# Kernel optimization log

Hardware: AMD Instinct MI355X
Metric: run time of the kernel (lower is better)

Reference implementation:

```python
import jax, jax.numpy as jnp
import numpy as np

N = 100000
E = 1600000
D = 128      # input feature dim
H = 128      # hidden_channels
O = 2        # out_channels
NEG_SLOPE = 0.2
EPS = 1e-16  # PyG softmax denominator epsilon


def gat_conv(x, src, dst, W_src, W_dst, att_src, att_dst, bias):
    """PyG GATConv, heads=1, add_self_loops=False, concat=True."""
    xs = x @ W_src                      # [N, C]
    xd = x @ W_dst                      # [N, C]
    a_s = xs @ att_src                  # [N]
    a_d = xd @ att_dst                  # [N]
    e = jax.nn.leaky_relu(a_s[src] + a_d[dst], NEG_SLOPE)   # [E]
    # segment softmax over edges grouped by destination node
    m = jax.ops.segment_max(e, dst, num_segments=N)          # [N]
    m = jnp.where(jnp.isfinite(m), m, 0.0)
    ex = jnp.exp(e - m[dst])                                  # [E]
    denom = jax.ops.segment_sum(ex, dst, num_segments=N)      # [N]
    alpha = ex / (denom[dst] + EPS)                            # [E]
    msg = alpha[:, None] * xs[src]                             # [E, C]
    out = jax.ops.segment_sum(msg, dst, num_segments=N)       # [N, C]
    return out + bias


def setup_inputs() -> dict:
    key = jax.random.key(0)
    ks = jax.random.split(key, 14)
    s = lambda k, shape, fan: jax.random.normal(k, shape, jnp.float32) * (1.0 / np.sqrt(fan))
    x = jax.random.normal(ks[0], (N, D), jnp.float32)
    edge_index = jax.random.randint(ks[1], (2, E), 0, N, dtype=jnp.int32)
    return {
        "x": x,
        "edge_index": edge_index,
        "W1s": s(ks[2], (D, H), D), "W1d": s(ks[3], (D, H), D),
        "a1s": s(ks[4], (H,), H),   "a1d": s(ks[5], (H,), H),
        "b1": jnp.zeros((H,), jnp.float32),
        "W2s": s(ks[6], (H, H), H), "W2d": s(ks[7], (H, H), H),
        "a2s": s(ks[8], (H,), H),   "a2d": s(ks[9], (H,), H),
        "b2": jnp.zeros((H,), jnp.float32),
        "Wl": s(ks[10], (H, O), H), "bl": jnp.zeros((O,), jnp.float32),
    }


def reference(x, edge_index, W1s, W1d, a1s, a1d, b1, W2s, W2d, a2s, a2d, b2, Wl, bl):
    src, dst = edge_index[0], edge_index[1]
    h = jax.nn.relu(gat_conv(x, src, dst, W1s, W1d, a1s, a1d, b1))
    # dropout p=0.3 is identity at inference
    h = jax.nn.relu(gat_conv(h, src, dst, W2s, W2d, a2s, a2d, b2))
    return h @ Wl + bl  # [N, O]
```

## Files before the change

kernel.cpp:

```cpp
#include <hip/hip_runtime.h>
#include <hip/hip_fp16.h>

#define NBSHIFT 8
#define BSZ     256
#define CAP     5120
#define EBLK    8192

typedef _Float16 f16x8 __attribute__((ext_vector_type(8)));
typedef float    f32x4 __attribute__((ext_vector_type(4)));


#define GEMM_LDS_BYTES (128 * 136 * 2 + 512)

template <bool XHALF>
__device__ __forceinline__ void gemm_body(
        const void* __restrict__ Xv, const float* __restrict__ Ws,
        const float* __restrict__ Wd, const float* __restrict__ attd,
        const float* __restrict__ att,
        __half* __restrict__ Y, float* __restrict__ a_s, float* __restrict__ a_d,
        int N, int blk, char* smem) {
    _Float16 (*sWh)[136] = (_Float16(*)[136])smem;
    float* svd = (float*)(smem + 128 * 136 * 2);
    int t = threadIdx.x;

    if (t < 128) {
        const float4* wr = (const float4*)&Wd[t * 128];
        const float4* ar = (const float4*)attd;
        float s = 0.f;
#pragma unroll 8
        for (int j = 0; j < 32; j++) {
            float4 w = wr[j], a = ar[j];
            s += w.x * a.x + w.y * a.y + w.z * a.z + w.w * a.w;
        }
        svd[t] = s;
    }
#pragma unroll
    for (int i = 0; i < 16; i++) {
        int gid = t + i * 256;
        int n = gid & 127, kq = gid >> 7;
        _Float16 p[4];
        p[0] = (_Float16)Ws[(kq * 4 + 0) * 128 + n];
        p[1] = (_Float16)Ws[(kq * 4 + 1) * 128 + n];
        p[2] = (_Float16)Ws[(kq * 4 + 2) * 128 + n];
        p[3] = (_Float16)Ws[(kq * 4 + 3) * 128 + n];
        *(uint2*)&sWh[n][kq * 4] = *(uint2*)p;
    }
    __syncthreads();

    int l = t & 63, wv = t >> 6;
    int quad = l >> 4, lm = l & 15;
    int rbase = blk * 64 + wv * 16;
    int arow = rbase + lm;
    bool rok = arow < N;

    f32x4 acc[8];
#pragma unroll
    for (int c = 0; c < 8; c++) acc[c] = (f32x4){0.f, 0.f, 0.f, 0.f};
    float adp = 0.f;

#pragma unroll
    for (int kc = 0; kc < 4; kc++) {
        int k0 = kc * 32 + quad * 8;
        float xf[8];
        f16x8 af;
        if constexpr (XHALF) {
            const __half* xrow = (const __half*)Xv + (size_t)arow * 128;
            if (rok) {
                af = *(const f16x8*)&xrow[k0];
            } else {
#pragma unroll
                for (int j = 0; j < 8; j++) af[j] = (_Float16)0.f;
            }
#pragma unroll
            for (int j = 0; j < 8; j++) xf[j] = (float)af[j];
        } else {
            const float* xrow = (const float*)Xv + (size_t)arow * 128;
            if (rok) {
                *(float4*)&xf[0] = *(const float4*)&xrow[k0];
                *(float4*)&xf[4] = *(const float4*)&xrow[k0 + 4];
            } else {
#pragma unroll
                for (int j = 0; j < 8; j++) xf[j] = 0.f;
            }
#pragma unroll
            for (int j = 0; j < 8; j++) af[j] = (_Float16)xf[j];
        }
        float4 v0 = *(const float4*)&svd[k0];
        float4 v1 = *(const float4*)&svd[k0 + 4];
        adp += xf[0] * v0.x + xf[1] * v0.y + xf[2] * v0.z + xf[3] * v0.w
             + xf[4] * v1.x + xf[5] * v1.y + xf[6] * v1.z + xf[7] * v1.w;
#pragma unroll
        for (int c = 0; c < 8; c++) {
            f16x8 bf = *(const f16x8*)&sWh[c * 16 + lm][k0];
            acc[c] = __builtin_amdgcn_mfma_f32_16x16x32_f16(af, bf, acc[c], 0, 0, 0);
        }
    }

    adp += __shfl_xor(adp, 16);
    adp += __shfl_xor(adp, 32);
    if (quad == 0 && rok) a_d[arow] = adp;

    float attc[8];
#pragma unroll
    for (int c = 0; c < 8; c++) attc[c] = att[c * 16 + lm];
#pragma unroll
    for (int r = 0; r < 4; r++) {
        int grow = rbase + quad * 4 + r;
        bool gok = grow < N;
        float p = 0.f;
#pragma unroll
        for (int c = 0; c < 8; c++) {
            if (gok) Y[(size_t)grow * 128 + c * 16 + lm] = __float2half(acc[c][r]);
            p += acc[c][r] * attc[c];
        }
        p += __shfl_xor(p, 1); p += __shfl_xor(p, 2); p += __shfl_xor(p, 4); p += __shfl_xor(p, 8);
        if (lm == 0 && gok) a_s[grow] = p;
    }
}

__global__ __launch_bounds__(256, 4) void k_fuse1(
        const float* __restrict__ X, const float* __restrict__ W1s,
        const float* __restrict__ W1d, const float* __restrict__ a1d,
        const float* __restrict__ a1s,
        __half* __restrict__ Y, float* __restrict__ a_s, float* __restrict__ a_d, int N, int gb,
        const int* __restrict__ src, const int* __restrict__ dst, int E,
        int* __restrict__ cursor, unsigned* __restrict__ pairs) {
    __shared__ __align__(16) char smem[GEMM_LDS_BYTES];
    int t = threadIdx.x;

    if ((int)blockIdx.x >= gb) {
        int* hist  = (int*)smem;
        int* start = hist + 512;
        hist[t] = 0; hist[t + 256] = 0;
        __syncthreads();
        int e00 = ((int)blockIdx.x - gb) * EBLK;

#pragma unroll
        for (int ch = 0; ch < EBLK / 1024; ch++) {
            int e = e00 + ch * 1024 + t * 4;
            if (e + 3 < E) {
                int4 dv = *(const int4*)&dst[e];
                atomicAdd(&hist[dv.x >> NBSHIFT], 1);
                atomicAdd(&hist[dv.y >> NBSHIFT], 1);
                atomicAdd(&hist[dv.z >> NBSHIFT], 1);
                atomicAdd(&hist[dv.w >> NBSHIFT], 1);
            } else {
                for (int i = 0; i < 4; i++)
                    if (e + i < E) atomicAdd(&hist[dst[e + i] >> NBSHIFT], 1);
            }
        }
        __syncthreads();
        if (hist[t] > 0)       start[t]       = atomicAdd(&cursor[t],       hist[t]);
        if (hist[t + 256] > 0) start[t + 256] = atomicAdd(&cursor[t + 256], hist[t + 256]);
        __syncthreads();
        hist[t] = 0; hist[t + 256] = 0;
        __syncthreads();
#pragma unroll
        for (int ch = 0; ch < EBLK / 1024; ch++) {
            int e = e00 + ch * 1024 + t * 4;
            if (e + 3 < E) {
                int4 dv = *(const int4*)&dst[e];
                int4 sv = *(const int4*)&src[e];
                int b0 = dv.x >> NBSHIFT; int r0 = atomicAdd(&hist[b0], 1);
                pairs[b0 * CAP + start[b0] + r0] = ((unsigned)(dv.x & (BSZ - 1)) << 17) | (unsigned)sv.x;
                int b1 = dv.y >> NBSHIFT; int r1 = atomicAdd(&hist[b1], 1);
                pairs[b1 * CAP + start[b1] + r1] = ((unsigned)(dv.y & (BSZ - 1)) << 17) | (unsigned)sv.y;
                int b2 = dv.z >> NBSHIFT; int r2 = atomicAdd(&hist[b2], 1);
                pairs[b2 * CAP + start[b2] + r2] = ((unsigned)(dv.z & (BSZ - 1)) << 17) | (unsigned)sv.z;
                int b3 = dv.w >> NBSHIFT; int r3 = atomicAdd(&hist[b3], 1);
                pairs[b3 * CAP + start[b3] + r3] = ((unsigned)(dv.w & (BSZ - 1)) << 17) | (unsigned)sv.w;
            } else {
                for (int i = 0; i < 4; i++) {
                    if (e + i < E) {
                        int d = dst[e + i], s = src[e + i];
                        int b = d >> NBSHIFT;
                        int r = atomicAdd(&hist[b], 1);
                        pairs[b * CAP + start[b] + r] = ((unsigned)(d & (BSZ - 1)) << 17) | (unsigned)s;
                    }
                }
            }
        }
        return;
    }

    gemm_body<false>(X, W1s, W1d, a1d, a1s, Y, a_s, a_d, N, blockIdx.x, smem);
}

__global__ __launch_bounds__(256, 4) void k_gemm2(
        const __half* __restrict__ X, const float* __restrict__ W2s,
        const float* __restrict__ W2d, const float* __restrict__ a2d,
        const float* __restrict__ a2s,
        __half* __restrict__ Y, float* __restrict__ a_s, float* __restrict__ a_d, int N) {
    __shared__ __align__(16) char smem[GEMM_LDS_BYTES];
    gemm_body<true>(X, W2s, W2d, a2d, a2s, Y, a_s, a_d, N, blockIdx.x, smem);
}

__global__ __launch_bounds__(256) void kB_csr(const unsigned* __restrict__ pairs,
                                              const int* __restrict__ cursor,
                                              int* __restrict__ row_start, int* __restrict__ row_end,
                                              int* __restrict__ csr_src, int N) {
    __shared__ int cnt[BSZ];
    __shared__ int cur[BSZ];
    __shared__ int sS[256];
    int b = blockIdx.x, t = threadIdx.x;
    int base = b * CAP;
    int ecnt = cursor[b];
    int nodeBase = b << NBSHIFT;
    cnt[t] = 0;
    __syncthreads();
    for (int j = t; j < ecnt; j += 256)
        atomicAdd(&cnt[pairs[base + j] >> 17], 1);
    __syncthreads();
    int c0 = cnt[t];
    sS[t] = c0; __syncthreads();
    for (int off = 1; off < 256; off <<= 1) {
        int x = (t >= off) ? sS[t - off] : 0;
        __syncthreads();
        sS[t] += x;
        __syncthreads();
    }
    int excl = sS[t] - c0;
    cur[t] = excl;
    int g = nodeBase + t;
    if (g < N) { row_start[g] = base + excl; row_end[g] = base + excl + c0; }
    __syncthreads();
    for (int j = t; j < ecnt; j += 256) {
        unsigned p = pairs[base + j];
        int r = atomicAdd(&cur[p >> 17], 1);
        csr_src[base + r] = (int)(p & 0x1FFFFu);
    }
}


__device__ __forceinline__ void fma_mix2(float& a0, float& a1, unsigned h2, float w) {
    asm("v_fma_mix_f32 %0, %1, %2, %0 op_sel_hi:[1,0,0]" : "+v"(a0) : "v"(h2), "v"(w));
    asm("v_fma_mix_f32 %0, %1, %2, %0 op_sel:[1,0,0] op_sel_hi:[1,0,0]" : "+v"(a1) : "v"(h2), "v"(w));
}

#define ACC_MIX(u, wj)  do {                                    \
    const unsigned* _w32 = (const unsigned*)&(u);               \
    fma_mix2(acc[0], acc[1], _w32[0], (wj));                    \
    fma_mix2(acc[2], acc[3], _w32[1], (wj));                    \
    fma_mix2(acc[4], acc[5], _w32[2], (wj));                    \
    fma_mix2(acc[6], acc[7], _w32[3], (wj));                    \
} while (0)

template <bool HEAD>
__global__ __launch_bounds__(256, 6) void k_agg(const int* __restrict__ csr_src, const int* __restrict__ rs_,
                                                const int* __restrict__ re_,
                                                const float* __restrict__ a_s, const float* __restrict__ a_d,
                                                const __half* __restrict__ xs, const float* __restrict__ bias,
                                                const float* __restrict__ Wl, const float* __restrict__ bl,
                                                void* __restrict__ outv, int N) {
    __shared__ int2 sP[4][4][16];
    int t = threadIdx.x; int wv = t >> 6, l = t & 63;
    int q = l >> 4, es = l & 15;
    int n = blockIdx.x * 16 + wv * 4 + q;
    bool nok = n < N;
    int rs0 = 0, deg = 0;
    if (nok) { rs0 = rs_[n]; deg = re_[n] - rs0; }
    float adn = nok ? a_d[n] : 0.f;
    const int* cs = csr_src + rs0;
    int c = es * 8;

    int R = (deg + 15) >> 4;
    R = max(R, __shfl_xor(R, 16));
    R = max(R, __shfl_xor(R, 32));

    float acc[8];
#pragma unroll
    for (int k = 0; k < 8; k++) acc[k] = 0.f;
    float dnl = 0.f;
    int2 (*sq)[16] = sP[wv];

    for (int r = 0; r < R; ++r) {
        int i = r * 16 + es;
        int idx = 0; float w = 0.f;
        if (i < deg) {
            idx = cs[i];
            float tv = a_s[idx] + adn;
            tv = tv > 0.f ? tv : 0.2f * tv;
            w = __expf(tv);
        }
        dnl += w;
        sq[q][es] = make_int2(idx, __float_as_int(w));

        int rem = deg - r * 16;
        int mcq = rem >= 16 ? 16 : (rem > 0 ? ((rem + 3) & ~3) : 0);
        const int2* spq = sq[q];
        for (int e = 0; e < mcq; e += 4) {
            int4 pA = *(const int4*)&spq[e];
            int4 pB = *(const int4*)&spq[e + 2];
            uint4 u0 = *(const uint4*)&xs[(size_t)pA.x * 128 + c];
            uint4 u1 = *(const uint4*)&xs[(size_t)pA.z * 128 + c];
            uint4 u2 = *(const uint4*)&xs[(size_t)pB.x * 128 + c];
            uint4 u3 = *(const uint4*)&xs[(size_t)pB.z * 128 + c];
            ACC_MIX(u0, __int_as_float(pA.y));
            ACC_MIX(u1, __int_as_float(pA.w));
            ACC_MIX(u2, __int_as_float(pB.y));
            ACC_MIX(u3, __int_as_float(pB.w));
        }
    }

    dnl += __shfl_xor(dnl, 1);
    dnl += __shfl_xor(dnl, 2);
    dnl += __shfl_xor(dnl, 4);
    dnl += __shfl_xor(dnl, 8);
    float inv = 1.f / (dnl + 1e-16f);

    float hv[8];
    float4 b0 = *(const float4*)&bias[c];
    float4 b1 = *(const float4*)&bias[c + 4];
    float bb[8] = {b0.x, b0.y, b0.z, b0.w, b1.x, b1.y, b1.z, b1.w};
#pragma unroll
    for (int k = 0; k < 8; k++) {
        float v = acc[k] * inv + bb[k];
        hv[k] = v > 0.f ? v : 0.f;
    }

    if (HEAD) {
        float p0 = 0.f, p1 = 0.f;
#pragma unroll
        for (int k = 0; k < 8; k++) {
            p0 += hv[k] * Wl[2 * (c + k)];
            p1 += hv[k] * Wl[2 * (c + k) + 1];
        }
        p0 += __shfl_xor(p0, 1); p0 += __shfl_xor(p0, 2);
        p0 += __shfl_xor(p0, 4); p0 += __shfl_xor(p0, 8);
        p1 += __shfl_xor(p1, 1); p1 += __shfl_xor(p1, 2);
        p1 += __shfl_xor(p1, 4); p1 += __shfl_xor(p1, 8);
        if (es == 0 && nok) {
            float* out = (float*)outv;
            out[2 * n]     = p0 + bl[0];
            out[2 * n + 1] = p1 + bl[1];
        }
    } else {
        if (nok) {
            __half* hout = (__half*)outv;
            __half hb[8];
#pragma unroll
            for (int k = 0; k < 8; k++) hb[k] = __float2half(hv[k]);
            *(uint4*)&hout[(size_t)n * 128 + c] = *(uint4*)hb;
        }
    }
}


extern "C" void kernel_launch(void* const* d_in, const int* in_sizes, int n_in,
                              void* d_out, int out_size, void* d_ws, size_t ws_size,
                              hipStream_t stream) {
    const float* x   = (const float*)d_in[0];
    const int*   ei  = (const int*)d_in[1];
    const float* W1s = (const float*)d_in[2];
    const float* W1d = (const float*)d_in[3];
    const float* a1s = (const float*)d_in[4];
    const float* a1d = (const float*)d_in[5];
    const float* b1  = (const float*)d_in[6];
    const float* W2s = (const float*)d_in[7];
    const float* W2d = (const float*)d_in[8];
    const float* a2s = (const float*)d_in[9];
    const float* a2d = (const float*)d_in[10];
    const float* b2  = (const float*)d_in[11];
    const float* Wl  = (const float*)d_in[12];
    const float* bl  = (const float*)d_in[13];
    float* out = (float*)d_out;

    int N = in_sizes[0] / 128;
    int E = in_sizes[1] / 2;
    const int* srcA = ei;
    const int* dstA = ei + E;
    int NB = (N + BSZ - 1) >> NBSHIFT;

    __half* xs = (__half*)d_ws;
    __half* h  = xs + (size_t)N * 128;
    float* as_ = (float*)(h + (size_t)N * 128);
    float* ad_ = as_ + N;
    int* row_start = (int*)(ad_ + N);
    int* row_end   = row_start + N;
    int* csr_src   = row_end + N;
    int* cursor    = csr_src + (size_t)NB * CAP;
    unsigned* pairs = (unsigned*)h;

    int gb = (N + 63) / 64;
    int EB = (E + EBLK - 1) / EBLK;
    int ab = (N + 15) / 16;

    hipMemsetAsync(cursor, 0, (size_t)NB * 4, stream);

    k_fuse1<<<gb + EB, 256, 0, stream>>>(x, W1s, W1d, a1d, a1s, xs, as_, ad_, N, gb,
                                         srcA, dstA, E, cursor, pairs);

    kB_csr<<<NB, 256, 0, stream>>>(pairs, cursor, row_start, row_end, csr_src, N);

    k_agg<false><<<ab, 256, 0, stream>>>(csr_src, row_start, row_end, as_, ad_, xs, b1, nullptr, nullptr, h, N);

    k_gemm2<<<gb, 256, 0, stream>>>(h, W2s, W2d, a2d, a2s, xs, as_, ad_, N);

    k_agg<true><<<ab, 256, 0, stream>>>(csr_src, row_start, row_end, as_, ad_, xs, b2, Wl, bl, out, N);
}
```

Before: 313.5 us.

## Split binning from GEMM1, prefetch GEMM inputs, unroll aggregation gathers

```diff
diff --git a/kernel.cpp b/kernel.cpp
--- a/kernel.cpp
+++ b/kernel.cpp
@@ -9,8 +9,17 @@
 typedef _Float16 f16x8 __attribute__((ext_vector_type(8)));
 typedef float    f32x4 __attribute__((ext_vector_type(4)));
 
-
 #define GEMM_LDS_BYTES (128 * 136 * 2 + 512)
+
+__device__ __forceinline__ f16x8 cvt_dot8(float4 x0, float4 x1, const float* sv, float& adp) {
+    f16x8 a;
+    a[0] = (_Float16)x0.x; a[1] = (_Float16)x0.y; a[2] = (_Float16)x0.z; a[3] = (_Float16)x0.w;
+    a[4] = (_Float16)x1.x; a[5] = (_Float16)x1.y; a[6] = (_Float16)x1.z; a[7] = (_Float16)x1.w;
+    float4 v0 = *(const float4*)sv, v1 = *(const float4*)(sv + 4);
+    adp += x0.x * v0.x + x0.y * v0.y + x0.z * v0.z + x0.w * v0.w
+         + x1.x * v1.x + x1.y * v1.y + x1.z * v1.z + x1.w * v1.w;
+    return a;
+}
 
 template <bool XHALF>
 __device__ __forceinline__ void gemm_body(
@@ -22,6 +31,35 @@
     _Float16 (*sWh)[136] = (_Float16(*)[136])smem;
     float* svd = (float*)(smem + 128 * 136 * 2);
     int t = threadIdx.x;
+    int l = t & 63, wv = t >> 6;
+    int quad = l >> 4, lm = l & 15;
+    int rbase = blk * 64 + wv * 16;
+    int arow = rbase + lm;
+    bool rok = arow < N;
+
+    float4 xf[8];
+    f16x8  xh[4];
+    if constexpr (XHALF) {
+        const f16x8* xr = (const f16x8*)((const __half*)Xv + (size_t)arow * 128 + quad * 8);
+        if (rok) { xh[0] = xr[0]; xh[1] = xr[4]; xh[2] = xr[8]; xh[3] = xr[12]; }
+        else {
+#pragma unroll
+            for (int kc = 0; kc < 4; kc++)
+#pragma unroll
+                for (int j = 0; j < 8; j++) xh[kc][j] = (_Float16)0.f;
+        }
+    } else {
+        const float4* xr = (const float4*)((const float*)Xv + (size_t)arow * 128 + quad * 8);
+        if (rok) {
+            xf[0] = xr[0];  xf[1] = xr[1];
+            xf[2] = xr[8];  xf[3] = xr[9];
+            xf[4] = xr[16]; xf[5] = xr[17];
+            xf[6] = xr[24]; xf[7] = xr[25];
+        } else {
+#pragma unroll
+            for (int j = 0; j < 8; j++) xf[j] = make_float4(0.f, 0.f, 0.f, 0.f);
+        }
+    }
 
     if (t < 128) {
         const float4* wr = (const float4*)&Wd[t * 128];
@@ -47,52 +85,33 @@
     }
     __syncthreads();
 
-    int l = t & 63, wv = t >> 6;
-    int quad = l >> 4, lm = l & 15;
-    int rbase = blk * 64 + wv * 16;
-    int arow = rbase + lm;
-    bool rok = arow < N;
+    float adp = 0.f;
+    f16x8 af[4];
+    if constexpr (XHALF) {
+#pragma unroll
+        for (int kc = 0; kc < 4; kc++) {
+            af[kc] = xh[kc];
+            const float* sv = &svd[kc * 32 + quad * 8];
+#pragma unroll
+            for (int j = 0; j < 8; j++) adp += (float)xh[kc][j] * sv[j];
+        }
+    } else {
+        af[0] = cvt_dot8(xf[0], xf[1], &svd[0  + quad * 8], adp);
+        af[1] = cvt_dot8(xf[2], xf[3], &svd[32 + quad * 8], adp);
+        af[2] = cvt_dot8(xf[4], xf[5], &svd[64 + quad * 8], adp);
+        af[3] = cvt_dot8(xf[6], xf[7], &svd[96 + quad * 8], adp);
+    }
 
     f32x4 acc[8];
 #pragma unroll
     for (int c = 0; c < 8; c++) acc[c] = (f32x4){0.f, 0.f, 0.f, 0.f};
-    float adp = 0.f;
-
 #pragma unroll
     for (int kc = 0; kc < 4; kc++) {
         int k0 = kc * 32 + quad * 8;
-        float xf[8];
-        f16x8 af;
-        if constexpr (XHALF) {
-            const __half* xrow = (const __half*)Xv + (size_t)arow * 128;
-            if (rok) {
-                af = *(const f16x8*)&xrow[k0];
-            } else {
-#pragma unroll
-                for (int j = 0; j < 8; j++) af[j] = (_Float16)0.f;
-            }
-#pragma unroll
-            for (int j = 0; j < 8; j++) xf[j] = (float)af[j];
-        } else {
-            const float* xrow = (const float*)Xv + (size_t)arow * 128;
-            if (rok) {
-                *(float4*)&xf[0] = *(const float4*)&xrow[k0];
-                *(float4*)&xf[4] = *(const float4*)&xrow[k0 + 4];
-            } else {
-#pragma unroll
-                for (int j = 0; j < 8; j++) xf[j] = 0.f;
-            }
-#pragma unroll
-            for (int j = 0; j < 8; j++) af[j] = (_Float16)xf[j];
-        }
-        float4 v0 = *(const float4*)&svd[k0];
-        float4 v1 = *(const float4*)&svd[k0 + 4];
-        adp += xf[0] * v0.x + xf[1] * v0.y + xf[2] * v0.z + xf[3] * v0.w
-             + xf[4] * v1.x + xf[5] * v1.y + xf[6] * v1.z + xf[7] * v1.w;
 #pragma unroll
         for (int c = 0; c < 8; c++) {
             f16x8 bf = *(const f16x8*)&sWh[c * 16 + lm][k0];
-            acc[c] = __builtin_amdgcn_mfma_f32_16x16x32_f16(af, bf, acc[c], 0, 0, 0);
+            acc[c] = __builtin_amdgcn_mfma_f32_16x16x32_f16(af[kc], bf, acc[c], 0, 0, 0);
         }
     }
 
@@ -118,71 +137,69 @@
     }
 }
 
-__global__ __launch_bounds__(256, 4) void k_fuse1(
+__global__ __launch_bounds__(256) void k_bin(
+        const int* __restrict__ src, const int* __restrict__ dst, int E,
+        int* __restrict__ cursor, unsigned* __restrict__ pairs) {
+    __shared__ int hist[512];
+    __shared__ int start[512];
+    int t = threadIdx.x;
+    hist[t] = 0; hist[t + 256] = 0;
+    __syncthreads();
+    int e00 = (int)blockIdx.x * EBLK;
+
+#pragma unroll
+    for (int ch = 0; ch < EBLK / 1024; ch++) {
+        int e = e00 + ch * 1024 + t * 4;
+        if (e + 3 < E) {
+            int4 dv = *(const int4*)&dst[e];
+            atomicAdd(&hist[dv.x >> NBSHIFT], 1);
+            atomicAdd(&hist[dv.y >> NBSHIFT], 1);
+            atomicAdd(&hist[dv.z >> NBSHIFT], 1);
+            atomicAdd(&hist[dv.w >> NBSHIFT], 1);
+        } else {
+            for (int i = 0; i < 4; i++)
+                if (e + i < E) atomicAdd(&hist[dst[e + i] >> NBSHIFT], 1);
+        }
+    }
+    __syncthreads();
+    if (hist[t] > 0)       start[t]       = atomicAdd(&cursor[t],       hist[t]);
+    if (hist[t + 256] > 0) start[t + 256] = atomicAdd(&cursor[t + 256], hist[t + 256]);
+    __syncthreads();
+    hist[t] = 0; hist[t + 256] = 0;
+    __syncthreads();
+#pragma unroll
+    for (int ch = 0; ch < EBLK / 1024; ch++) {
+        int e = e00 + ch * 1024 + t * 4;
+        if (e + 3 < E) {
+            int4 dv = *(const int4*)&dst[e];
+            int4 sv = *(const int4*)&src[e];
+            int b0 = dv.x >> NBSHIFT; int r0 = atomicAdd(&hist[b0], 1);
+            pairs[b0 * CAP + start[b0] + r0] = ((unsigned)(dv.x & (BSZ - 1)) << 17) | (unsigned)sv.x;
+            int b1 = dv.y >> NBSHIFT; int r1 = atomicAdd(&hist[b1], 1);
+            pairs[b1 * CAP + start[b1] + r1] = ((unsigned)(dv.y & (BSZ - 1)) << 17) | (unsigned)sv.y;
+            int b2 = dv.z >> NBSHIFT; int r2 = atomicAdd(&hist[b2], 1);
+            pairs[b2 * CAP + start[b2] + r2] = ((unsigned)(dv.z & (BSZ - 1)) << 17) | (unsigned)sv.z;
+            int b3 = dv.w >> NBSHIFT; int r3 = atomicAdd(&hist[b3], 1);
+            pairs[b3 * CAP + start[b3] + r3] = ((unsigned)(dv.w & (BSZ - 1)) << 17) | (unsigned)sv.w;
+        } else {
+            for (int i = 0; i < 4; i++) {
+                if (e + i < E) {
+                    int d = dst[e + i], s = src[e + i];
+                    int b = d >> NBSHIFT;
+                    int r = atomicAdd(&hist[b], 1);
+                    pairs[b * CAP + start[b] + r] = ((unsigned)(d & (BSZ - 1)) << 17) | (unsigned)s;
+                }
+            }
+        }
+    }
+}
+
+__global__ __launch_bounds__(256, 4) void k_gemm1(
         const float* __restrict__ X, const float* __restrict__ W1s,
         const float* __restrict__ W1d, const float* __restrict__ a1d,
         const float* __restrict__ a1s,
-        __half* __restrict__ Y, float* __restrict__ a_s, float* __restrict__ a_d, int N, int gb,
-        const int* __restrict__ src, const int* __restrict__ dst, int E,
-        int* __restrict__ cursor, unsigned* __restrict__ pairs) {
+        __half* __restrict__ Y, float* __restrict__ a_s, float* __restrict__ a_d, int N) {
     __shared__ __align__(16) char smem[GEMM_LDS_BYTES];
-    int t = threadIdx.x;
-
-    if ((int)blockIdx.x >= gb) {
-        int* hist  = (int*)smem;
-        int* start = hist + 512;
-        hist[t] = 0; hist[t + 256] = 0;
-        __syncthreads();
-        int e00 = ((int)blockIdx.x - gb) * EBLK;
-
-#pragma unroll
-        for (int ch = 0; ch < EBLK / 1024; ch++) {
-            int e = e00 + ch * 1024 + t * 4;
-            if (e + 3 < E) {
-                int4 dv = *(const int4*)&dst[e];
-                atomicAdd(&hist[dv.x >> NBSHIFT], 1);
-                atomicAdd(&hist[dv.y >> NBSHIFT], 1);
-                atomicAdd(&hist[dv.z >> NBSHIFT], 1);
-                atomicAdd(&hist[dv.w >> NBSHIFT], 1);
-            } else {
-                for (int i = 0; i < 4; i++)
-                    if (e + i < E) atomicAdd(&hist[dst[e + i] >> NBSHIFT], 1);
-            }
-        }
-        __syncthreads();
-        if (hist[t] > 0)       start[t]       = atomicAdd(&cursor[t],       hist[t]);
-        if (hist[t + 256] > 0) start[t + 256] = atomicAdd(&cursor[t + 256], hist[t + 256]);
-        __syncthreads();
-        hist[t] = 0; hist[t + 256] = 0;
-        __syncthreads();
-#pragma unroll
-        for (int ch = 0; ch < EBLK / 1024; ch++) {
-            int e = e00 + ch * 1024 + t * 4;
-            if (e + 3 < E) {
-                int4 dv = *(const int4*)&dst[e];
-                int4 sv = *(const int4*)&src[e];
-                int b0 = dv.x >> NBSHIFT; int r0 = atomicAdd(&hist[b0], 1);
-                pairs[b0 * CAP + start[b0] + r0] = ((unsigned)(dv.x & (BSZ - 1)) << 17) | (unsigned)sv.x;
-                int b1 = dv.y >> NBSHIFT; int r1 = atomicAdd(&hist[b1], 1);
-                pairs[b1 * CAP + start[b1] + r1] = ((unsigned)(dv.y & (BSZ - 1)) << 17) | (unsigned)sv.y;
-                int b2 = dv.z >> NBSHIFT; int r2 = atomicAdd(&hist[b2], 1);
-                pairs[b2 * CAP + start[b2] + r2] = ((unsigned)(dv.z & (BSZ - 1)) << 17) | (unsigned)sv.z;
-                int b3 = dv.w >> NBSHIFT; int r3 = atomicAdd(&hist[b3], 1);
-                pairs[b3 * CAP + start[b3] + r3] = ((unsigned)(dv.w & (BSZ - 1)) << 17) | (unsigned)sv.w;
-            } else {
-                for (int i = 0; i < 4; i++) {
-                    if (e + i < E) {
-                        int d = dst[e + i], s = src[e + i];
-                        int b = d >> NBSHIFT;
-                        int r = atomicAdd(&hist[b], 1);
-                        pairs[b * CAP + start[b] + r] = ((unsigned)(d & (BSZ - 1)) << 17) | (unsigned)s;
-                    }
-                }
-            }
-        }
-        return;
-    }
-
     gemm_body<false>(X, W1s, W1d, a1d, a1s, Y, a_s, a_d, N, blockIdx.x, smem);
 }
 
@@ -245,8 +262,22 @@
     fma_mix2(acc[6], acc[7], _w32[3], (wj));                    \
 } while (0)
 
+#define GATHER4(u0, u1, u2, u3, pa, pb)  do {                   \
+    u0 = *(const uint4*)&xs[(size_t)(pa).x * 128 + c];          \
+    u1 = *(const uint4*)&xs[(size_t)(pa).z * 128 + c];          \
+    u2 = *(const uint4*)&xs[(size_t)(pb).x * 128 + c];          \
+    u3 = *(const uint4*)&xs[(size_t)(pb).z * 128 + c];          \
+} while (0)
+
+#define CONSUME4(u0, u1, u2, u3, pa, pb)  do {                  \
+    ACC_MIX(u0, __int_as_float((pa).y));                        \
+    ACC_MIX(u1, __int_as_float((pa).w));                        \
+    ACC_MIX(u2, __int_as_float((pb).y));                        \
+    ACC_MIX(u3, __int_as_float((pb).w));                        \
+} while (0)
+
 template <bool HEAD>
-__global__ __launch_bounds__(256, 6) void k_agg(const int* __restrict__ csr_src, const int* __restrict__ rs_,
+__global__ __launch_bounds__(256, 5) void k_agg(const int* __restrict__ csr_src, const int* __restrict__ rs_,
                                                 const int* __restrict__ re_,
                                                 const float* __restrict__ a_s, const float* __restrict__ a_d,
                                                 const __half* __restrict__ xs, const float* __restrict__ bias,
@@ -272,6 +303,7 @@
     for (int k = 0; k < 8; k++) acc[k] = 0.f;
     float dnl = 0.f;
     int2 (*sq)[16] = sP[wv];
+    const int2* spq = sq[q];
 
     for (int r = 0; r < R; ++r) {
         int i = r * 16 + es;
@@ -285,21 +317,23 @@
         dnl += w;
         sq[q][es] = make_int2(idx, __float_as_int(w));
 
-        int rem = deg - r * 16;
-        int mcq = rem >= 16 ? 16 : (rem > 0 ? ((rem + 3) & ~3) : 0);
-        const int2* spq = sq[q];
-        for (int e = 0; e < mcq; e += 4) {
-            int4 pA = *(const int4*)&spq[e];
-            int4 pB = *(const int4*)&spq[e + 2];
-            uint4 u0 = *(const uint4*)&xs[(size_t)pA.x * 128 + c];
-            uint4 u1 = *(const uint4*)&xs[(size_t)pA.z * 128 + c];
-            uint4 u2 = *(const uint4*)&xs[(size_t)pB.x * 128 + c];
-            uint4 u3 = *(const uint4*)&xs[(size_t)pB.z * 128 + c];
-            ACC_MIX(u0, __int_as_float(pA.y));
-            ACC_MIX(u1, __int_as_float(pA.w));
-            ACC_MIX(u2, __int_as_float(pB.y));
-            ACC_MIX(u3, __int_as_float(pB.w));
-        }
+        int4 pa0 = *(const int4*)&spq[0],  pb0 = *(const int4*)&spq[2];
+        uint4 u00, u01, u02, u03;
+        GATHER4(u00, u01, u02, u03, pa0, pb0);
+        int4 pa1 = *(const int4*)&spq[4],  pb1 = *(const int4*)&spq[6];
+        uint4 u10, u11, u12, u13;
+        GATHER4(u10, u11, u12, u13, pa1, pb1);
+
+        CONSUME4(u00, u01, u02, u03, pa0, pb0);
+        pa0 = *(const int4*)&spq[8]; pb0 = *(const int4*)&spq[10];
+        GATHER4(u00, u01, u02, u03, pa0, pb0);
+
+        CONSUME4(u10, u11, u12, u13, pa1, pb1);
+        pa1 = *(const int4*)&spq[12]; pb1 = *(const int4*)&spq[14];
+        GATHER4(u10, u11, u12, u13, pa1, pb1);
+
+        CONSUME4(u00, u01, u02, u03, pa0, pb0);
+        CONSUME4(u10, u11, u12, u13, pa1, pb1);
     }
 
     dnl += __shfl_xor(dnl, 1);
@@ -387,8 +421,9 @@
 
     hipMemsetAsync(cursor, 0, (size_t)NB * 4, stream);
 
-    k_fuse1<<<gb + EB, 256, 0, stream>>>(x, W1s, W1d, a1d, a1s, xs, as_, ad_, N, gb,
-                                         srcA, dstA, E, cursor, pairs);
+    k_bin<<<EB, 256, 0, stream>>>(srcA, dstA, E, cursor, pairs);
+
+    k_gemm1<<<gb, 256, 0, stream>>>(x, W1s, W1d, a1d, a1s, xs, as_, ad_, N);
 
     kB_csr<<<NB, 256, 0, stream>>>(pairs, cursor, row_start, row_end, csr_src, N);
 
```

Measured after the change: 327.5 us. +4.5%, slower.

## Process four row groups per GEMM block and privatize CSR histogram per wave

Applied to the files above, without the earlier changes.

```diff
diff --git a/kernel.cpp b/kernel.cpp
--- a/kernel.cpp
+++ b/kernel.cpp
@@ -5,10 +5,10 @@
 #define BSZ     256
 #define CAP     5120
 #define EBLK    8192
+#define ROWG    4
 
 typedef _Float16 f16x8 __attribute__((ext_vector_type(8)));
 typedef float    f32x4 __attribute__((ext_vector_type(4)));
-
 
 #define GEMM_LDS_BYTES (128 * 136 * 2 + 512)
 
@@ -49,72 +49,85 @@
 
     int l = t & 63, wv = t >> 6;
     int quad = l >> 4, lm = l & 15;
-    int rbase = blk * 64 + wv * 16;
-    int arow = rbase + lm;
-    bool rok = arow < N;
-
-    f32x4 acc[8];
-#pragma unroll
-    for (int c = 0; c < 8; c++) acc[c] = (f32x4){0.f, 0.f, 0.f, 0.f};
-    float adp = 0.f;
-
-#pragma unroll
-    for (int kc = 0; kc < 4; kc++) {
-        int k0 = kc * 32 + quad * 8;
-        float xf[8];
-        f16x8 af;
+
+    float attc[8];
+#pragma unroll
+    for (int c = 0; c < 8; c++) attc[c] = att[c * 16 + lm];
+
+#pragma unroll
+    for (int g = 0; g < ROWG; ++g) {
+        int rbase = blk * (64 * ROWG) + g * 64 + wv * 16;
+        int arow = rbase + lm;
+        bool rok = arow < N;
+
+        float adp = 0.f;
+        f16x8 af[4];
         if constexpr (XHALF) {
             const __half* xrow = (const __half*)Xv + (size_t)arow * 128;
-            if (rok) {
-                af = *(const f16x8*)&xrow[k0];
-            } else {
-#pragma unroll
-                for (int j = 0; j < 8; j++) af[j] = (_Float16)0.f;
-            }
-#pragma unroll
-            for (int j = 0; j < 8; j++) xf[j] = (float)af[j];
+#pragma unroll
+            for (int kc = 0; kc < 4; kc++) {
+                int k0 = kc * 32 + quad * 8;
+                if (rok) af[kc] = *(const f16x8*)&xrow[k0];
+                else {
+#pragma unroll
+                    for (int j = 0; j < 8; j++) af[kc][j] = (_Float16)0.f;
+                }
+                const float* sv = &svd[k0];
+#pragma unroll
+                for (int j = 0; j < 8; j++) adp += (float)af[kc][j] * sv[j];
+            }
         } else {
             const float* xrow = (const float*)Xv + (size_t)arow * 128;
-            if (rok) {
-                *(float4*)&xf[0] = *(const float4*)&xrow[k0];
-                *(float4*)&xf[4] = *(const float4*)&xrow[k0 + 4];
-            } else {
-#pragma unroll
-                for (int j = 0; j < 8; j++) xf[j] = 0.f;
-            }
-#pragma unroll
-            for (int j = 0; j < 8; j++) af[j] = (_Float16)xf[j];
-        }
-        float4 v0 = *(const float4*)&svd[k0];
-        float4 v1 = *(const float4*)&svd[k0 + 4];
-        adp += xf[0] * v0.x + xf[1] * v0.y + xf[2] * v0.z + xf[3] * v0.w
-             + xf[4] * v1.x + xf[5] * v1.y + xf[6] * v1.z + xf[7] * v1.w;
-#pragma unroll
-        for (int c = 0; c < 8; c++) {
-            f16x8 bf = *(const f16x8*)&sWh[c * 16 + lm][k0];
-            acc[c] = __builtin_amdgcn_mfma_f32_16x16x32_f16(af, bf, acc[c], 0, 0, 0);
-        }
-    }
-
-    adp += __shfl_xor(adp, 16);
-    adp += __shfl_xor(adp, 32);
-    if (quad == 0 && rok) a_d[arow] = adp;
-
-    float attc[8];
-#pragma unroll
-    for (int c = 0; c < 8; c++) attc[c] = att[c * 16 + lm];
-#pragma unroll
-    for (int r = 0; r < 4; r++) {
-        int grow = rbase + quad * 4 + r;
-        bool gok = grow < N;
-        float p = 0.f;
-#pragma unroll
-        for (int c = 0; c < 8; c++) {
-            if (gok) Y[(size_t)grow * 128 + c * 16 + lm] = __float2half(acc[c][r]);
-            p += acc[c][r] * attc[c];
-        }
-        p += __shfl_xor(p, 1); p += __shfl_xor(p, 2); p += __shfl_xor(p, 4); p += __shfl_xor(p, 8);
-        if (lm == 0 && gok) a_s[grow] = p;
+#pragma unroll
+            for (int kc = 0; kc < 4; kc++) {
+                int k0 = kc * 32 + quad * 8;
+                float xf[8];
+                if (rok) {
+                    *(float4*)&xf[0] = *(const float4*)&xrow[k0];
+                    *(float4*)&xf[4] = *(const float4*)&xrow[k0 + 4];
+                } else {
+#pragma unroll
+                    for (int j = 0; j < 8; j++) xf[j] = 0.f;
+                }
+                float4 v0 = *(const float4*)&svd[k0];
+                float4 v1 = *(const float4*)&svd[k0 + 4];
+                adp += xf[0] * v0.x + xf[1] * v0.y + xf[2] * v0.z + xf[3] * v0.w
+                     + xf[4] * v1.x + xf[5] * v1.y + xf[6] * v1.z + xf[7] * v1.w;
+#pragma unroll
+                for (int j = 0; j < 8; j++) af[kc][j] = (_Float16)xf[j];
+            }
+        }
+
+        f32x4 acc[8];
+#pragma unroll
+        for (int c = 0; c < 8; c++) acc[c] = (f32x4){0.f, 0.f, 0.f, 0.f};
+#pragma unroll
+        for (int kc = 0; kc < 4; kc++) {
+            int k0 = kc * 32 + quad * 8;
+#pragma unroll
+            for (int c = 0; c < 8; c++) {
+                f16x8 bf = *(const f16x8*)&sWh[c * 16 + lm][k0];
+                acc[c] = __builtin_amdgcn_mfma_f32_16x16x32_f16(af[kc], bf, acc[c], 0, 0, 0);
+            }
+        }
+
+        adp += __shfl_xor(adp, 16);
+        adp += __shfl_xor(adp, 32);
+        if (quad == 0 && rok) a_d[arow] = adp;
+
+#pragma unroll
+        for (int r = 0; r < 4; r++) {
+            int grow = rbase + quad * 4 + r;
+            bool gok = grow < N;
+            float p = 0.f;
+#pragma unroll
+            for (int c = 0; c < 8; c++) {
+                if (gok) Y[(size_t)grow * 128 + c * 16 + lm] = __float2half(acc[c][r]);
+                p += acc[c][r] * attc[c];
+            }
+            p += __shfl_xor(p, 1); p += __shfl_xor(p, 2); p += __shfl_xor(p, 4); p += __shfl_xor(p, 8);
+            if (lm == 0 && gok) a_s[grow] = p;
+        }
     }
 }
 
@@ -199,19 +212,21 @@
                                               const int* __restrict__ cursor,
                                               int* __restrict__ row_start, int* __restrict__ row_end,
                                               int* __restrict__ csr_src, int N) {
-    __shared__ int cnt[BSZ];
+    __shared__ int cnt4[4][BSZ];
     __shared__ int cur[BSZ];
     __shared__ int sS[256];
     int b = blockIdx.x, t = threadIdx.x;
+    int wv = t >> 6;
     int base = b * CAP;
     int ecnt = cursor[b];
     int nodeBase = b << NBSHIFT;
-    cnt[t] = 0;
+#pragma unroll
+    for (int k = 0; k < 4; k++) cnt4[k][t] = 0;
     __syncthreads();
     for (int j = t; j < ecnt; j += 256)
-        atomicAdd(&cnt[pairs[base + j] >> 17], 1);
+        atomicAdd(&cnt4[wv][pairs[base + j] >> 17], 1);
     __syncthreads();
-    int c0 = cnt[t];
+    int c0 = cnt4[0][t] + cnt4[1][t] + cnt4[2][t] + cnt4[3][t];
     sS[t] = c0; __syncthreads();
     for (int off = 1; off < 256; off <<= 1) {
         int x = (t >= off) ? sS[t - off] : 0;
@@ -381,7 +396,7 @@
     int* cursor    = csr_src + (size_t)NB * CAP;
     unsigned* pairs = (unsigned*)h;
 
-    int gb = (N + 63) / 64;
+    int gb = (N + 64 * ROWG - 1) / (64 * ROWG);
     int EB = (E + EBLK - 1) / EBLK;
     int ab = (N + 15) / 16;
 
```

After: 363.4 us. 1.16x slower.
